# Performance work log

Measured on AMD Instinct MI355X. Metric: run time of the kernel, lower is better.

The kernel has to match this reference:

```python
import jax, jax.numpy as jnp
import numpy as np

D_IN, D_H, D_G, H, B = 512, 256, 128, 8, 4096
EPS_LN = 1e-6
EPS_STD = 1e-6


def setup_inputs() -> dict:
    key = jax.random.key(0)
    ks = jax.random.split(key, 4)
    x = jax.random.normal(ks[0], (B, D_IN), dtype=jnp.float32)
    # Dense params (flax kernel layout: (in, out)), lecun-normal-ish init
    Wh = jax.random.normal(ks[1], (D_IN, D_H), dtype=jnp.float32) / np.sqrt(D_IN)
    bh = jnp.zeros((D_H,), dtype=jnp.float32)
    Wz1 = jax.random.normal(ks[2], (D_IN, H * D_H), dtype=jnp.float32) / np.sqrt(D_IN)
    Wz2 = jax.random.normal(ks[3], (D_IN, H * D_G), dtype=jnp.float32) / np.sqrt(D_IN)
    ln_scale = jnp.ones((D_H,), dtype=jnp.float32)
    ln_bias = jnp.zeros((D_H,), dtype=jnp.float32)
    return {"x": x, "Wh": Wh, "bh": bh, "Wz1": Wz1, "Wz2": Wz2,
            "ln_scale": ln_scale, "ln_bias": ln_bias}


def _layer_norm(a, scale, bias):
    mu = jnp.mean(a, axis=-1, keepdims=True)
    var = jnp.var(a, axis=-1, keepdims=True)
    return (a - mu) * jax.lax.rsqrt(var + EPS_LN) * scale + bias


def reference(x, Wh, bh, Wz1, Wz2, ln_scale, ln_bias):
    sz_b = x.shape[0]
    # h: (B, d_h)
    h = _layer_norm(jax.nn.relu(x @ Wh + bh), ln_scale, ln_bias)
    z1 = (x @ Wz1).reshape(sz_b, H, D_H)   # (B, H, d_h)
    z2 = (x @ Wz2).reshape(sz_b, H, D_G)   # (B, H, d_g)
    # w = z2^T @ z1 over heads: (B, d_g, d_h)
    w = jnp.einsum('bhg,bhd->bgd', z2, z1)
    # per-row standardization (population std, ddof=0) + tanh
    mu = jnp.mean(w, axis=-1, keepdims=True)
    sd = jnp.std(w, axis=-1, keepdims=True)
    w = jnp.tanh((w - mu) / (sd + EPS_STD))
    # y = w @ h: (B, d_g)
    y = jnp.einsum('bgd,bd->bg', w, h)
    return h, y
```

## Files before the change

kernel.cpp:

```cpp
#include <hip/hip_runtime.h>
#include <hip/hip_bf16.h>
#include <cstdint>

#define BATCH 4096
#define DIN   512
#define DH    256
#define DG    128
#define NH    8
#define NTOT  3328
#define S2    264

typedef __bf16 bf16x8 __attribute__((ext_vector_type(8)));
typedef float  f32x4  __attribute__((ext_vector_type(4)));

__device__ __forceinline__ unsigned short f2bf(float f) {
    union { float f; uint32_t u; } v; v.f = f;
    uint32_t u = v.u;
    u += 0x7fffu + ((u >> 16) & 1u);
    return (unsigned short)(u >> 16);
}
__device__ __forceinline__ float bf2f(unsigned short s) {
    union { uint32_t u; float f; } v; v.u = ((uint32_t)s) << 16;
    return v.f;
}

__device__ __forceinline__ void async16(const unsigned short* g, unsigned short* l) {
    __builtin_amdgcn_global_load_lds(
        (const __attribute__((address_space(1))) unsigned int*)(uintptr_t)g,
        (__attribute__((address_space(3))) unsigned int*)(uintptr_t)l,
        16, 0, 0);
}

__global__ __launch_bounds__(256) void prep_kernel(const float* __restrict__ x,
                                                   const float* __restrict__ Wh,
                                                   const float* __restrict__ Wz1,
                                                   const float* __restrict__ Wz2,
                                                   unsigned short* __restrict__ xb,
                                                   unsigned short* __restrict__ Wt) {
    __shared__ float tile[32][33];
    int bid = blockIdx.x;
    int t = threadIdx.x;
    if (bid < 2048) {
        int i = (bid * 256 + t) * 4;
        float4 v = *(const float4*)(x + i);
        ushort4 o;
        o.x = f2bf(v.x); o.y = f2bf(v.y); o.z = f2bf(v.z); o.w = f2bf(v.w);
        *(ushort4*)(xb + i) = o;
        return;
    }
    int b2 = bid - 2048;
    int n0 = (b2 % 104) * 32;
    int k0 = (b2 / 104) * 32;
    const float* W; int ldn, nl;
    if (n0 < 256)       { W = Wh;  ldn = 256;  nl = n0; }
    else if (n0 < 2304) { W = Wz1; ldn = 2048; nl = n0 - 256; }
    else                { W = Wz2; ldn = 1024; nl = n0 - 2304; }
    int tx = t & 31, ty = t >> 5;
    #pragma unroll
    for (int i = 0; i < 4; i++) {
        int kk = ty + i * 8;
        tile[kk][tx] = W[(size_t)(k0 + kk) * ldn + nl + tx];
    }
    __syncthreads();
    #pragma unroll
    for (int i = 0; i < 4; i++) {
        int nn = ty + i * 8;
        Wt[(size_t)(n0 + nn) * 512 + k0 + tx] = f2bf(tile[tx][nn]);
    }
}

__global__ __launch_bounds__(256) void gemm_kernel(const unsigned short* __restrict__ xb,
                                                   const unsigned short* __restrict__ Wt,
                                                   unsigned short* __restrict__ Zb) {
    __shared__ unsigned short As[128 * 64];
    __shared__ unsigned short Bs[128 * 64];
    const int m0 = blockIdx.y * 128;
    const int n0 = blockIdx.x * 128;
    const int t = threadIdx.x;
    const int w = t >> 6, lane = t & 63;
    const int wm = (w >> 1) * 64, wn = (w & 1) * 64;
    const int lrow = lane & 15, q = lane >> 4;

    f32x4 acc[4][4] = {};

    for (int k0 = 0; k0 < DIN; k0 += 64) {
        __syncthreads();
        #pragma unroll
        for (int j = 0; j < 4; j++) {
            int gidx = (w * 4 + j) * 64 + lane;
            int row = gidx >> 3, slot = gidx & 7;
            int src = slot ^ (row & 7);
            const unsigned short* ga = xb + (size_t)(m0 + row) * DIN + k0 + src * 8;
            const unsigned short* gb = Wt + (size_t)(n0 + row) * DIN + k0 + src * 8;
            async16(ga, As + (w * 4 + j) * 512);
            async16(gb, Bs + (w * 4 + j) * 512);
        }
        __syncthreads();
        #pragma unroll
        for (int ks = 0; ks < 2; ks++) {
            bf16x8 af[4], bfr[4];
            #pragma unroll
            for (int i = 0; i < 4; i++) {
                int row = wm + i * 16 + lrow;
                int phys = (ks * 4 + q) ^ (row & 7);
                af[i] = *reinterpret_cast<const bf16x8*>(As + row * 64 + phys * 8);
            }
            #pragma unroll
            for (int j = 0; j < 4; j++) {
                int row = wn + j * 16 + lrow;
                int phys = (ks * 4 + q) ^ (row & 7);
                bfr[j] = *reinterpret_cast<const bf16x8*>(Bs + row * 64 + phys * 8);
            }
            #pragma unroll
            for (int i = 0; i < 4; i++)
                #pragma unroll
                for (int j = 0; j < 4; j++)
                    acc[i][j] = __builtin_amdgcn_mfma_f32_16x16x32_bf16(af[i], bfr[j], acc[i][j], 0, 0, 0);
        }
    }
    #pragma unroll
    for (int i = 0; i < 4; i++)
        #pragma unroll
        for (int j = 0; j < 4; j++) {
            int col = n0 + wn + j * 16 + lrow;
            int rbase = m0 + wm + i * 16 + q * 4;
            #pragma unroll
            for (int r = 0; r < 4; r++)
                Zb[(size_t)(rbase + r) * NTOT + col] = f2bf(acc[i][j][r]);
        }
}

__global__ __launch_bounds__(256) void attn_kernel(const unsigned short* __restrict__ Zb,
                                                   const float* __restrict__ bh,
                                                   const float* __restrict__ lns,
                                                   const float* __restrict__ lnb,
                                                   float* __restrict__ h_out,
                                                   float* __restrict__ y_out) {
    __shared__ unsigned short z1s[16 * S2];
    __shared__ unsigned short z2s[NH * DG];
    __shared__ unsigned short z1cb[DH * 8];
    __shared__ unsigned short z2A[DG * 8];
    __shared__ unsigned short zpad[8];
    __shared__ float hs[DH];
    __shared__ float GL[9][9];
    __shared__ float red[4][3];
    const int b = blockIdx.x;
    const int t = threadIdx.x;
    const int wv = t >> 6, lane = t & 63;
    const int lrow = lane & 15, q = lane >> 4;
    const unsigned short* Zrow = Zb + (size_t)b * NTOT;

    {
        uint4 v1 = *(const uint4*)(Zrow + 256 + t * 8);
        *(uint4*)(z1s + (t >> 5) * S2 + (t & 31) * 8) = v1;
        if (t < 128) {
            uint4 v2 = *(const uint4*)(Zrow + 2304 + t * 8);
            *(uint4*)(z2s + t * 8) = v2;
        }
        z1s[8 * S2 + t] = 0x3F80;
        if (t < 8) zpad[t] = 0;
    }
    float v = fmaxf(bf2f(Zrow[t]) + bh[t], 0.0f);
    float s = v, sq = v * v;
    #pragma unroll
    for (int m = 32; m >= 1; m >>= 1) {
        s  += __shfl_xor(s,  m, 64);
        sq += __shfl_xor(sq, m, 64);
    }
    if (lane == 0) { red[wv][0] = s; red[wv][1] = sq; }
    __syncthreads();

    if (wv == 3) {
        f32x4 g = {};
        #pragma unroll
        for (int ks = 0; ks < 8; ks++) {
            bf16x8 fr = *reinterpret_cast<const bf16x8*>(z1s + lrow * S2 + ks * 32 + q * 8);
            g = __builtin_amdgcn_mfma_f32_16x16x32_bf16(fr, fr, g, 0, 0, 0);
        }
        #pragma unroll
        for (int r = 0; r < 4; r++) {
            int row = q * 4 + r;
            if (row < 9 && lrow < 9) GL[row][lrow] = g[r];
        }
    }
    {
        float ss = red[0][0] + red[1][0] + red[2][0] + red[3][0];
        float qq = red[0][1] + red[1][1] + red[2][1] + red[3][1];
        float mu  = ss * (1.0f / 256.0f);
        float var = qq * (1.0f / 256.0f) - mu * mu;
        float hval = (v - mu) * rsqrtf(var + 1e-6f) * lns[t] + lnb[t];
        hs[t] = hval;
        h_out[(size_t)b * DH + t] = hval;
        float hp = hval;
        #pragma unroll
        for (int m = 32; m >= 1; m >>= 1) hp += __shfl_xor(hp, m, 64);
        if (lane == 0) red[wv][2] = hp;
    }
    __syncthreads();

    {
        unsigned short pk[8];
        #pragma unroll
        for (int h = 0; h < NH; h++) {
            float c = bf2f(z1s[h * S2 + t]) - GL[h][8] * (1.0f / 256.0f);
            pk[h] = f2bf(c);
        }
        ushort4 lo = {pk[0], pk[1], pk[2], pk[3]};
        ushort4 hi = {pk[4], pk[5], pk[6], pk[7]};
        *(ushort4*)(z1cb + t * 8)     = lo;
        *(ushort4*)(z1cb + t * 8 + 4) = hi;
    }
    if (t < DG) {
        float z2g[NH];
        #pragma unroll
        for (int h = 0; h < NH; h++) z2g[h] = bf2f(z2s[h * DG + t]);
        float mug = 0.f, qg = 0.f;
        #pragma unroll
        for (int h = 0; h < NH; h++) {
            mug += z2g[h] * GL[h][8];
            float inn = 0.f;
            #pragma unroll
            for (int h2 = 0; h2 < NH; h2++) inn += z2g[h2] * GL[h][h2];
            qg += z2g[h] * inn;
        }
        mug *= (1.0f / 256.0f);
        qg  *= (1.0f / 256.0f);
        float vg = fmaxf(qg - mug * mug, 0.0f);
        float A = 2.0f * 1.4426950408889634f / (sqrtf(vg) + 1e-6f);
        unsigned short pk[8];
        #pragma unroll
        for (int h = 0; h < NH; h++) pk[h] = f2bf(z2g[h] * A);
        ushort4 lo = {pk[0], pk[1], pk[2], pk[3]};
        ushort4 hi = {pk[4], pk[5], pk[6], pk[7]};
        *(ushort4*)(z2A + t * 8)     = lo;
        *(ushort4*)(z2A + t * 8 + 4) = hi;
    }
    __syncthreads();

    const unsigned short* bptr = (q == 0) ? (z1cb + lrow * 8) : zpad;
    const int binc = (q == 0) ? 128 : 0;
    bf16x8 af[2];
    #pragma unroll
    for (int gt = 0; gt < 2; gt++) {
        const unsigned short* aptr = (q == 0) ? (z2A + (wv * 32 + gt * 16 + lrow) * 8) : zpad;
        af[gt] = *reinterpret_cast<const bf16x8*>(aptr);
    }
    float hv[16];
    #pragma unroll
    for (int dt = 0; dt < 16; dt++) hv[dt] = hs[dt * 16 + lrow];

    f32x4 czero = {};
    float yn[2][4] = {};
    #pragma unroll 4
    for (int dt = 0; dt < 16; dt++) {
        bf16x8 bfr = *reinterpret_cast<const bf16x8*>(bptr + dt * binc);
        #pragma unroll
        for (int gt = 0; gt < 2; gt++) {
            f32x4 c = __builtin_amdgcn_mfma_f32_16x16x32_bf16(af[gt], bfr, czero, 0, 0, 0);
            #pragma unroll
            for (int r = 0; r < 4; r++) {
                float e = __builtin_amdgcn_exp2f(c[r]);
                yn[gt][r] = fmaf(hv[dt], __builtin_amdgcn_rcpf(e + 1.0f), yn[gt][r]);
            }
        }
    }
    #pragma unroll
    for (int m = 1; m <= 8; m <<= 1)
        #pragma unroll
        for (int gt = 0; gt < 2; gt++)
            #pragma unroll
            for (int r = 0; r < 4; r++)
                yn[gt][r] += __shfl_xor(yn[gt][r], m, 64);
    if (lrow == 0) {
        float Hsum = red[0][2] + red[1][2] + red[2][2] + red[3][2];
        #pragma unroll
        for (int gt = 0; gt < 2; gt++)
            #pragma unroll
            for (int r = 0; r < 4; r++)
                y_out[(size_t)b * DG + wv * 32 + gt * 16 + q * 4 + r] = Hsum - 2.0f * yn[gt][r];
    }
}

extern "C" void kernel_launch(void* const* d_in, const int* in_sizes, int n_in,
                              void* d_out, int out_size, void* d_ws, size_t ws_size,
                              hipStream_t stream) {
    const float* x   = (const float*)d_in[0];
    const float* Wh  = (const float*)d_in[1];
    const float* bh  = (const float*)d_in[2];
    const float* Wz1 = (const float*)d_in[3];
    const float* Wz2 = (const float*)d_in[4];
    const float* lns = (const float*)d_in[5];
    const float* lnb = (const float*)d_in[6];
    float* h_out = (float*)d_out;
    float* y_out = h_out + (size_t)BATCH * DH;

    char* ws = (char*)d_ws;
    unsigned short* Zb = (unsigned short*)ws;
    unsigned short* xb = (unsigned short*)(ws + 27262976);
    unsigned short* Wt = (unsigned short*)(ws + 31457280);

    prep_kernel<<<3712, 256, 0, stream>>>(x, Wh, Wz1, Wz2, xb, Wt);
    gemm_kernel<<<dim3(NTOT / 128, BATCH / 128), 256, 0, stream>>>(xb, Wt, Zb);
    attn_kernel<<<BATCH, 256, 0, stream>>>(Zb, bh, lns, lnb, h_out, y_out);
}
```

Baseline: 144.1 us.

## Process eight batch rows per attention block with one wave per row pair

New measurement: 142.3 us. No clear change (-1.2%).

```diff
diff --git a/kernel.cpp b/kernel.cpp
--- a/kernel.cpp
+++ b/kernel.cpp
@@ -8,7 +8,9 @@
 #define DG    128
 #define NH    8
 #define NTOT  3328
-#define S2    264
+#define RPB   8
+#define SH    264
+#define RREG  (9 * SH)
 
 typedef __bf16 bf16x8 __attribute__((ext_vector_type(8)));
 typedef float  f32x4  __attribute__((ext_vector_type(4)));
@@ -130,154 +132,214 @@
         }
 }
 
-__global__ __launch_bounds__(256) void attn_kernel(const unsigned short* __restrict__ Zb,
-                                                   const float* __restrict__ bh,
-                                                   const float* __restrict__ lns,
-                                                   const float* __restrict__ lnb,
-                                                   float* __restrict__ h_out,
-                                                   float* __restrict__ y_out) {
-    __shared__ unsigned short z1s[16 * S2];
-    __shared__ unsigned short z2s[NH * DG];
-    __shared__ unsigned short z1cb[DH * 8];
-    __shared__ unsigned short z2A[DG * 8];
-    __shared__ unsigned short zpad[8];
-    __shared__ float hs[DH];
-    __shared__ float GL[9][9];
-    __shared__ float red[4][3];
-    const int b = blockIdx.x;
+__global__ __launch_bounds__(256, 2) void attn_kernel(const unsigned short* __restrict__ Zb,
+                                                      const float* __restrict__ bh,
+                                                      const float* __restrict__ lns,
+                                                      const float* __restrict__ lnb,
+                                                      float* __restrict__ h_out,
+                                                      float* __restrict__ y_out) {
+    __shared__ __align__(16) unsigned short z1a[RPB * RREG + 7 * SH];
+    __shared__ __align__(16) unsigned short z2b[RPB * 1024];
+    __shared__ __align__(16) float hsr[RPB][DH];
+    __shared__ float GLr[RPB][9][9];
+    __shared__ float redH[RPB];
+    __shared__ __align__(16) unsigned short zpad[8];
+    const int b0 = blockIdx.x * RPB;
     const int t = threadIdx.x;
     const int wv = t >> 6, lane = t & 63;
     const int lrow = lane & 15, q = lane >> 4;
-    const unsigned short* Zrow = Zb + (size_t)b * NTOT;
+
+    #pragma unroll
+    for (int r = 0; r < RPB; r++) {
+        const unsigned short* Zr = Zb + (size_t)(b0 + r) * NTOT;
+        uint4 v = *(const uint4*)(Zr + 256 + t * 8);
+        *(uint4*)(z1a + r * RREG + (t >> 5) * SH + (t & 31) * 8) = v;
+        z1a[r * RREG + 8 * SH + t] = 0x3F80;
+    }
+    #pragma unroll
+    for (int i = 0; i < 4; i++) {
+        int idx = i * 256 + t;
+        int r = idx >> 7, c = idx & 127;
+        uint4 v = *(const uint4*)(Zb + (size_t)(b0 + r) * NTOT + 2304 + c * 8);
+        *(uint4*)(z2b + r * 1024 + c * 8) = v;
+    }
+    if (t < 8) zpad[t] = 0;
 
     {
-        uint4 v1 = *(const uint4*)(Zrow + 256 + t * 8);
-        *(uint4*)(z1s + (t >> 5) * S2 + (t & 31) * 8) = v1;
-        if (t < 128) {
-            uint4 v2 = *(const uint4*)(Zrow + 2304 + t * 8);
-            *(uint4*)(z2s + t * 8) = v2;
-        }
-        z1s[8 * S2 + t] = 0x3F80;
-        if (t < 8) zpad[t] = 0;
-    }
-    float v = fmaxf(bf2f(Zrow[t]) + bh[t], 0.0f);
-    float s = v, sq = v * v;
-    #pragma unroll
-    for (int m = 32; m >= 1; m >>= 1) {
-        s  += __shfl_xor(s,  m, 64);
-        sq += __shfl_xor(sq, m, 64);
-    }
-    if (lane == 0) { red[wv][0] = s; red[wv][1] = sq; }
-    __syncthreads();
-
-    if (wv == 3) {
+        int r = t >> 5, d0 = (t & 31) * 8;
+        const unsigned short* Zr = Zb + (size_t)(b0 + r) * NTOT;
+        uint4 hp4 = *(const uint4*)(Zr + d0);
+        unsigned short hu[8];
+        *(uint4*)hu = hp4;
+        float4 ba = *(const float4*)(bh + d0);
+        float4 bb = *(const float4*)(bh + d0 + 4);
+        float vv[8];
+        vv[0] = fmaxf(bf2f(hu[0]) + ba.x, 0.f); vv[1] = fmaxf(bf2f(hu[1]) + ba.y, 0.f);
+        vv[2] = fmaxf(bf2f(hu[2]) + ba.z, 0.f); vv[3] = fmaxf(bf2f(hu[3]) + ba.w, 0.f);
+        vv[4] = fmaxf(bf2f(hu[4]) + bb.x, 0.f); vv[5] = fmaxf(bf2f(hu[5]) + bb.y, 0.f);
+        vv[6] = fmaxf(bf2f(hu[6]) + bb.z, 0.f); vv[7] = fmaxf(bf2f(hu[7]) + bb.w, 0.f);
+        float s = 0.f, sq = 0.f;
+        #pragma unroll
+        for (int i = 0; i < 8; i++) { s += vv[i]; sq += vv[i] * vv[i]; }
+        #pragma unroll
+        for (int m = 16; m >= 1; m >>= 1) {
+            s  += __shfl_xor(s,  m, 64);
+            sq += __shfl_xor(sq, m, 64);
+        }
+        float mu  = s * (1.0f / 256.0f);
+        float var = sq * (1.0f / 256.0f) - mu * mu;
+        float rs = rsqrtf(var + 1e-6f);
+        float4 la = *(const float4*)(lns + d0);
+        float4 lb = *(const float4*)(lns + d0 + 4);
+        float4 oa = *(const float4*)(lnb + d0);
+        float4 ob = *(const float4*)(lnb + d0 + 4);
+        float hvv[8];
+        hvv[0] = (vv[0] - mu) * rs * la.x + oa.x; hvv[1] = (vv[1] - mu) * rs * la.y + oa.y;
+        hvv[2] = (vv[2] - mu) * rs * la.z + oa.z; hvv[3] = (vv[3] - mu) * rs * la.w + oa.w;
+        hvv[4] = (vv[4] - mu) * rs * lb.x + ob.x; hvv[5] = (vv[5] - mu) * rs * lb.y + ob.y;
+        hvv[6] = (vv[6] - mu) * rs * lb.z + ob.z; hvv[7] = (vv[7] - mu) * rs * lb.w + ob.w;
+        *(float4*)(&hsr[r][d0])     = float4{hvv[0], hvv[1], hvv[2], hvv[3]};
+        *(float4*)(&hsr[r][d0 + 4]) = float4{hvv[4], hvv[5], hvv[6], hvv[7]};
+        float* ho = h_out + (size_t)(b0 + r) * DH + d0;
+        *(float4*)ho       = float4{hvv[0], hvv[1], hvv[2], hvv[3]};
+        *(float4*)(ho + 4) = float4{hvv[4], hvv[5], hvv[6], hvv[7]};
+        float hp = 0.f;
+        #pragma unroll
+        for (int i = 0; i < 8; i++) hp += hvv[i];
+        #pragma unroll
+        for (int m = 16; m >= 1; m >>= 1) hp += __shfl_xor(hp, m, 64);
+        if ((t & 31) == 0) redH[r] = hp;
+    }
+    __syncthreads();
+
+    #pragma unroll
+    for (int rr = 0; rr < 2; rr++) {
+        int r = wv * 2 + rr;
         f32x4 g = {};
         #pragma unroll
         for (int ks = 0; ks < 8; ks++) {
-            bf16x8 fr = *reinterpret_cast<const bf16x8*>(z1s + lrow * S2 + ks * 32 + q * 8);
+            bf16x8 fr = *reinterpret_cast<const bf16x8*>(z1a + r * RREG + lrow * SH + ks * 32 + q * 8);
             g = __builtin_amdgcn_mfma_f32_16x16x32_bf16(fr, fr, g, 0, 0, 0);
         }
         #pragma unroll
-        for (int r = 0; r < 4; r++) {
-            int row = q * 4 + r;
-            if (row < 9 && lrow < 9) GL[row][lrow] = g[r];
-        }
-    }
+        for (int i = 0; i < 4; i++) {
+            int crow = q * 4 + i;
+            if (crow < 9 && lrow < 9) GLr[r][crow][lrow] = g[i];
+        }
+    }
+    uint32_t pr[8][4];
     {
-        float ss = red[0][0] + red[1][0] + red[2][0] + red[3][0];
-        float qq = red[0][1] + red[1][1] + red[2][1] + red[3][1];
-        float mu  = ss * (1.0f / 256.0f);
-        float var = qq * (1.0f / 256.0f) - mu * mu;
-        float hval = (v - mu) * rsqrtf(var + 1e-6f) * lns[t] + lnb[t];
-        hs[t] = hval;
-        h_out[(size_t)b * DH + t] = hval;
-        float hp = hval;
-        #pragma unroll
-        for (int m = 32; m >= 1; m >>= 1) hp += __shfl_xor(hp, m, 64);
-        if (lane == 0) red[wv][2] = hp;
+        int r = t >> 5, la = t & 31;
+        float mh[8];
+        #pragma unroll
+        for (int h = 0; h < NH; h++) mh[h] = GLr[r][h][8] * (1.0f / 256.0f);
+        #pragma unroll
+        for (int jj = 0; jj < 8; jj++) {
+            int d = la + 32 * jj;
+            #pragma unroll
+            for (int h2 = 0; h2 < 4; h2++) {
+                float c0 = bf2f(z1a[r * RREG + (2 * h2) * SH + d])     - mh[2 * h2];
+                float c1 = bf2f(z1a[r * RREG + (2 * h2 + 1) * SH + d]) - mh[2 * h2 + 1];
+                pr[jj][h2] = (uint32_t)f2bf(c0) | ((uint32_t)f2bf(c1) << 16);
+            }
+        }
     }
     __syncthreads();
 
     {
-        unsigned short pk[8];
+        int r = t >> 5, la = t & 31;
+        #pragma unroll
+        for (int jj = 0; jj < 8; jj++) {
+            int d = la + 32 * jj;
+            *(uint4*)(z1a + r * RREG + d * 8) = uint4{pr[jj][0], pr[jj][1], pr[jj][2], pr[jj][3]};
+        }
+    }
+    uint32_t ps[4][4];
+    #pragma unroll
+    for (int i = 0; i < 4; i++) {
+        int idx = i * 256 + t;
+        int r = idx >> 7, g = idx & 127;
+        float z2g[NH];
+        #pragma unroll
+        for (int h = 0; h < NH; h++) z2g[h] = bf2f(z2b[r * 1024 + h * 128 + g]);
+        float mug = 0.f, qg = 0.f;
         #pragma unroll
         for (int h = 0; h < NH; h++) {
-            float c = bf2f(z1s[h * S2 + t]) - GL[h][8] * (1.0f / 256.0f);
-            pk[h] = f2bf(c);
-        }
-        ushort4 lo = {pk[0], pk[1], pk[2], pk[3]};
-        ushort4 hi = {pk[4], pk[5], pk[6], pk[7]};
-        *(ushort4*)(z1cb + t * 8)     = lo;
-        *(ushort4*)(z1cb + t * 8 + 4) = hi;
-    }
-    if (t < DG) {
-        float z2g[NH];
-        #pragma unroll
-        for (int h = 0; h < NH; h++) z2g[h] = bf2f(z2s[h * DG + t]);
-        float mug = 0.f, qg = 0.f;
-        #pragma unroll
-        for (int h = 0; h < NH; h++) {
-            mug += z2g[h] * GL[h][8];
+            mug += z2g[h] * GLr[r][h][8];
             float inn = 0.f;
             #pragma unroll
-            for (int h2 = 0; h2 < NH; h2++) inn += z2g[h2] * GL[h][h2];
+            for (int h2 = 0; h2 < NH; h2++) inn += z2g[h2] * GLr[r][h][h2];
             qg += z2g[h] * inn;
         }
         mug *= (1.0f / 256.0f);
         qg  *= (1.0f / 256.0f);
         float vg = fmaxf(qg - mug * mug, 0.0f);
         float A = 2.0f * 1.4426950408889634f / (sqrtf(vg) + 1e-6f);
-        unsigned short pk[8];
-        #pragma unroll
-        for (int h = 0; h < NH; h++) pk[h] = f2bf(z2g[h] * A);
-        ushort4 lo = {pk[0], pk[1], pk[2], pk[3]};
-        ushort4 hi = {pk[4], pk[5], pk[6], pk[7]};
-        *(ushort4*)(z2A + t * 8)     = lo;
-        *(ushort4*)(z2A + t * 8 + 4) = hi;
-    }
-    __syncthreads();
-
-    const unsigned short* bptr = (q == 0) ? (z1cb + lrow * 8) : zpad;
+        #pragma unroll
+        for (int h2 = 0; h2 < 4; h2++)
+            ps[i][h2] = (uint32_t)f2bf(z2g[2 * h2] * A) | ((uint32_t)f2bf(z2g[2 * h2 + 1] * A) << 16);
+    }
+    __syncthreads();
+
+    #pragma unroll
+    for (int i = 0; i < 4; i++) {
+        int idx = i * 256 + t;
+        int r = idx >> 7, g = idx & 127;
+        *(uint4*)(z2b + r * 1024 + g * 8) = uint4{ps[i][0], ps[i][1], ps[i][2], ps[i][3]};
+    }
+    __syncthreads();
+
+    const int ra = wv * 2, rb = wv * 2 + 1;
+    const unsigned short* bpA = (q == 0) ? (z1a + ra * RREG + lrow * 8) : zpad;
+    const unsigned short* bpB = (q == 0) ? (z1a + rb * RREG + lrow * 8) : zpad;
     const int binc = (q == 0) ? 128 : 0;
-    bf16x8 af[2];
-    #pragma unroll
-    for (int gt = 0; gt < 2; gt++) {
-        const unsigned short* aptr = (q == 0) ? (z2A + (wv * 32 + gt * 16 + lrow) * 8) : zpad;
-        af[gt] = *reinterpret_cast<const bf16x8*>(aptr);
-    }
-    float hv[16];
-    #pragma unroll
-    for (int dt = 0; dt < 16; dt++) hv[dt] = hs[dt * 16 + lrow];
-
+    bf16x8 afA[8], afB[8];
+    #pragma unroll
+    for (int gt = 0; gt < 8; gt++) {
+        const unsigned short* pa = (q == 0) ? (z2b + ra * 1024 + (gt * 16 + lrow) * 8) : zpad;
+        const unsigned short* pb = (q == 0) ? (z2b + rb * 1024 + (gt * 16 + lrow) * 8) : zpad;
+        afA[gt] = *reinterpret_cast<const bf16x8*>(pa);
+        afB[gt] = *reinterpret_cast<const bf16x8*>(pb);
+    }
     f32x4 czero = {};
-    float yn[2][4] = {};
-    #pragma unroll 4
+    float ynA[8][4] = {}, ynB[8][4] = {};
+    #pragma unroll 2
     for (int dt = 0; dt < 16; dt++) {
-        bf16x8 bfr = *reinterpret_cast<const bf16x8*>(bptr + dt * binc);
-        #pragma unroll
-        for (int gt = 0; gt < 2; gt++) {
-            f32x4 c = __builtin_amdgcn_mfma_f32_16x16x32_bf16(af[gt], bfr, czero, 0, 0, 0);
-            #pragma unroll
-            for (int r = 0; r < 4; r++) {
-                float e = __builtin_amdgcn_exp2f(c[r]);
-                yn[gt][r] = fmaf(hv[dt], __builtin_amdgcn_rcpf(e + 1.0f), yn[gt][r]);
+        bf16x8 bA = *reinterpret_cast<const bf16x8*>(bpA + dt * binc);
+        bf16x8 bB = *reinterpret_cast<const bf16x8*>(bpB + dt * binc);
+        float hvA = hsr[ra][dt * 16 + lrow];
+        float hvB = hsr[rb][dt * 16 + lrow];
+        #pragma unroll
+        for (int gt = 0; gt < 8; gt++) {
+            f32x4 cA = __builtin_amdgcn_mfma_f32_16x16x32_bf16(afA[gt], bA, czero, 0, 0, 0);
+            f32x4 cB = __builtin_amdgcn_mfma_f32_16x16x32_bf16(afB[gt], bB, czero, 0, 0, 0);
+            #pragma unroll
+            for (int r4 = 0; r4 < 4; r4++) {
+                float eA = __builtin_amdgcn_exp2f(cA[r4]);
+                ynA[gt][r4] = fmaf(hvA, __builtin_amdgcn_rcpf(eA + 1.0f), ynA[gt][r4]);
+                float eB = __builtin_amdgcn_exp2f(cB[r4]);
+                ynB[gt][r4] = fmaf(hvB, __builtin_amdgcn_rcpf(eB + 1.0f), ynB[gt][r4]);
             }
         }
     }
     #pragma unroll
     for (int m = 1; m <= 8; m <<= 1)
         #pragma unroll
-        for (int gt = 0; gt < 2; gt++)
-            #pragma unroll
-            for (int r = 0; r < 4; r++)
-                yn[gt][r] += __shfl_xor(yn[gt][r], m, 64);
+        for (int gt = 0; gt < 8; gt++)
+            #pragma unroll
+            for (int r4 = 0; r4 < 4; r4++) {
+                ynA[gt][r4] += __shfl_xor(ynA[gt][r4], m, 64);
+                ynB[gt][r4] += __shfl_xor(ynB[gt][r4], m, 64);
+            }
     if (lrow == 0) {
-        float Hsum = red[0][2] + red[1][2] + red[2][2] + red[3][2];
-        #pragma unroll
-        for (int gt = 0; gt < 2; gt++)
-            #pragma unroll
-            for (int r = 0; r < 4; r++)
-                y_out[(size_t)b * DG + wv * 32 + gt * 16 + q * 4 + r] = Hsum - 2.0f * yn[gt][r];
+        float HsA = redH[ra], HsB = redH[rb];
+        #pragma unroll
+        for (int gt = 0; gt < 8; gt++)
+            #pragma unroll
+            for (int r4 = 0; r4 < 4; r4++) {
+                y_out[(size_t)(b0 + ra) * DG + gt * 16 + q * 4 + r4] = HsA - 2.0f * ynA[gt][r4];
+                y_out[(size_t)(b0 + rb) * DG + gt * 16 + q * 4 + r4] = HsB - 2.0f * ynB[gt][r4];
+            }
     }
 }
 
@@ -301,5 +363,5 @@
 
     prep_kernel<<<3712, 256, 0, stream>>>(x, Wh, Wz1, Wz2, xb, Wt);
     gemm_kernel<<<dim3(NTOT / 128, BATCH / 128), 256, 0, stream>>>(xb, Wt, Zb);
-    attn_kernel<<<BATCH, 256, 0, stream>>>(Zb, bh, lns, lnb, h_out, y_out);
-}
+    attn_kernel<<<BATCH / RPB, 256, 0, stream>>>(Zb, bh, lns, lnb, h_out, y_out);
+}
```

## Process two batch rows per block in attn kernel with reworked work split

Applied to the files above, without the earlier changes.

After: 145.6 us. Within noise of the previous version (+1.0%).

```diff
diff --git a/kernel.cpp b/kernel.cpp
--- a/kernel.cpp
+++ b/kernel.cpp
@@ -8,7 +8,9 @@
 #define DG    128
 #define NH    8
 #define NTOT  3328
-#define S2    264
+#define RPB   2
+#define SH    264
+#define RREG  (9 * SH)
 
 typedef __bf16 bf16x8 __attribute__((ext_vector_type(8)));
 typedef float  f32x4  __attribute__((ext_vector_type(4)));
@@ -130,154 +132,175 @@
         }
 }
 
-__global__ __launch_bounds__(256) void attn_kernel(const unsigned short* __restrict__ Zb,
-                                                   const float* __restrict__ bh,
-                                                   const float* __restrict__ lns,
-                                                   const float* __restrict__ lnb,
-                                                   float* __restrict__ h_out,
-                                                   float* __restrict__ y_out) {
-    __shared__ unsigned short z1s[16 * S2];
-    __shared__ unsigned short z2s[NH * DG];
-    __shared__ unsigned short z1cb[DH * 8];
-    __shared__ unsigned short z2A[DG * 8];
-    __shared__ unsigned short zpad[8];
-    __shared__ float hs[DH];
-    __shared__ float GL[9][9];
-    __shared__ float red[4][3];
-    const int b = blockIdx.x;
+__global__ __launch_bounds__(256, 8) void attn_kernel(const unsigned short* __restrict__ Zb,
+                                                      const float* __restrict__ bh,
+                                                      const float* __restrict__ lns,
+                                                      const float* __restrict__ lnb,
+                                                      float* __restrict__ h_out,
+                                                      float* __restrict__ y_out) {
+    __shared__ __align__(16) unsigned short z1a[RPB * RREG + 7 * SH];
+    __shared__ __align__(16) unsigned short z2b[RPB * 1024];
+    __shared__ __align__(16) float hsr[RPB][DH];
+    __shared__ float GLr[RPB][9][9];
+    __shared__ float redH[RPB];
+    __shared__ __align__(16) unsigned short zpad[8];
+    const int b0 = blockIdx.x * RPB;
     const int t = threadIdx.x;
     const int wv = t >> 6, lane = t & 63;
     const int lrow = lane & 15, q = lane >> 4;
-    const unsigned short* Zrow = Zb + (size_t)b * NTOT;
-
+
+    #pragma unroll
+    for (int r = 0; r < RPB; r++) {
+        uint4 v = *(const uint4*)(Zb + (size_t)(b0 + r) * NTOT + 256 + t * 8);
+        *(uint4*)(z1a + r * RREG + (t >> 5) * SH + (t & 31) * 8) = v;
+        z1a[r * RREG + 8 * SH + t] = 0x3F80;
+    }
     {
-        uint4 v1 = *(const uint4*)(Zrow + 256 + t * 8);
-        *(uint4*)(z1s + (t >> 5) * S2 + (t & 31) * 8) = v1;
-        if (t < 128) {
-            uint4 v2 = *(const uint4*)(Zrow + 2304 + t * 8);
-            *(uint4*)(z2s + t * 8) = v2;
-        }
-        z1s[8 * S2 + t] = 0x3F80;
-        if (t < 8) zpad[t] = 0;
-    }
-    float v = fmaxf(bf2f(Zrow[t]) + bh[t], 0.0f);
-    float s = v, sq = v * v;
-    #pragma unroll
-    for (int m = 32; m >= 1; m >>= 1) {
-        s  += __shfl_xor(s,  m, 64);
-        sq += __shfl_xor(sq, m, 64);
-    }
-    if (lane == 0) { red[wv][0] = s; red[wv][1] = sq; }
-    __syncthreads();
-
-    if (wv == 3) {
+        int r = t >> 7, c = t & 127;
+        uint4 v = *(const uint4*)(Zb + (size_t)(b0 + r) * NTOT + 2304 + c * 8);
+        *(uint4*)(z2b + r * 1024 + c * 8) = v;
+    }
+    if (t < 8) zpad[t] = 0;
+
+    if (wv < 2) {
+        int r = wv, d0 = lane * 4;
+        const unsigned short* Zr = Zb + (size_t)(b0 + r) * NTOT;
+        ushort4 hu = *(const ushort4*)(Zr + d0);
+        float4 bv = *(const float4*)(bh + d0);
+        float vv[4];
+        vv[0] = fmaxf(bf2f(hu.x) + bv.x, 0.f);
+        vv[1] = fmaxf(bf2f(hu.y) + bv.y, 0.f);
+        vv[2] = fmaxf(bf2f(hu.z) + bv.z, 0.f);
+        vv[3] = fmaxf(bf2f(hu.w) + bv.w, 0.f);
+        float s = vv[0] + vv[1] + vv[2] + vv[3];
+        float sq = vv[0] * vv[0] + vv[1] * vv[1] + vv[2] * vv[2] + vv[3] * vv[3];
+        #pragma unroll
+        for (int m = 32; m >= 1; m >>= 1) {
+            s  += __shfl_xor(s,  m, 64);
+            sq += __shfl_xor(sq, m, 64);
+        }
+        float mu  = s * (1.0f / 256.0f);
+        float var = sq * (1.0f / 256.0f) - mu * mu;
+        float rs = rsqrtf(var + 1e-6f);
+        float4 lv = *(const float4*)(lns + d0);
+        float4 ov = *(const float4*)(lnb + d0);
+        float hv0 = (vv[0] - mu) * rs * lv.x + ov.x;
+        float hv1 = (vv[1] - mu) * rs * lv.y + ov.y;
+        float hv2 = (vv[2] - mu) * rs * lv.z + ov.z;
+        float hv3 = (vv[3] - mu) * rs * lv.w + ov.w;
+        *(float4*)(&hsr[r][d0]) = float4{hv0, hv1, hv2, hv3};
+        *(float4*)(h_out + (size_t)(b0 + r) * DH + d0) = float4{hv0, hv1, hv2, hv3};
+        float hp = hv0 + hv1 + hv2 + hv3;
+        #pragma unroll
+        for (int m = 32; m >= 1; m >>= 1) hp += __shfl_xor(hp, m, 64);
+        if (lane == 0) redH[r] = hp;
+    }
+    __syncthreads();
+
+    if (wv < 2) {
+        int r = wv;
         f32x4 g = {};
         #pragma unroll
         for (int ks = 0; ks < 8; ks++) {
-            bf16x8 fr = *reinterpret_cast<const bf16x8*>(z1s + lrow * S2 + ks * 32 + q * 8);
+            bf16x8 fr = *reinterpret_cast<const bf16x8*>(z1a + r * RREG + lrow * SH + ks * 32 + q * 8);
             g = __builtin_amdgcn_mfma_f32_16x16x32_bf16(fr, fr, g, 0, 0, 0);
         }
         #pragma unroll
-        for (int r = 0; r < 4; r++) {
-            int row = q * 4 + r;
-            if (row < 9 && lrow < 9) GL[row][lrow] = g[r];
-        }
-    }
+        for (int i = 0; i < 4; i++) {
+            int crow = q * 4 + i;
+            if (crow < 9 && lrow < 9) GLr[r][crow][lrow] = g[i];
+        }
+    }
+    const int sr = t >> 7, sg = t & 127;
+    float z2g[NH];
+    #pragma unroll
+    for (int h = 0; h < NH; h++) z2g[h] = bf2f(z2b[sr * 1024 + h * 128 + sg]);
+    __syncthreads();
+
+    uint32_t pr[2][4];
     {
-        float ss = red[0][0] + red[1][0] + red[2][0] + red[3][0];
-        float qq = red[0][1] + red[1][1] + red[2][1] + red[3][1];
-        float mu  = ss * (1.0f / 256.0f);
-        float var = qq * (1.0f / 256.0f) - mu * mu;
-        float hval = (v - mu) * rsqrtf(var + 1e-6f) * lns[t] + lnb[t];
-        hs[t] = hval;
-        h_out[(size_t)b * DH + t] = hval;
-        float hp = hval;
-        #pragma unroll
-        for (int m = 32; m >= 1; m >>= 1) hp += __shfl_xor(hp, m, 64);
-        if (lane == 0) red[wv][2] = hp;
-    }
-    __syncthreads();
-
+        float mh[NH];
+        #pragma unroll
+        for (int h = 0; h < NH; h++) mh[h] = GLr[sr][h][8] * (1.0f / 256.0f);
+        #pragma unroll
+        for (int it = 0; it < 2; it++) {
+            int d = (t & 127) + it * 128;
+            #pragma unroll
+            for (int h2 = 0; h2 < 4; h2++) {
+                float c0 = bf2f(z1a[sr * RREG + (2 * h2) * SH + d])     - mh[2 * h2];
+                float c1 = bf2f(z1a[sr * RREG + (2 * h2 + 1) * SH + d]) - mh[2 * h2 + 1];
+                pr[it][h2] = (uint32_t)f2bf(c0) | ((uint32_t)f2bf(c1) << 16);
+            }
+        }
+    }
+    uint32_t ps[4];
     {
-        unsigned short pk[8];
+        float mug = 0.f, qg = 0.f;
         #pragma unroll
         for (int h = 0; h < NH; h++) {
-            float c = bf2f(z1s[h * S2 + t]) - GL[h][8] * (1.0f / 256.0f);
-            pk[h] = f2bf(c);
-        }
-        ushort4 lo = {pk[0], pk[1], pk[2], pk[3]};
-        ushort4 hi = {pk[4], pk[5], pk[6], pk[7]};
-        *(ushort4*)(z1cb + t * 8)     = lo;
-        *(ushort4*)(z1cb + t * 8 + 4) = hi;
-    }
-    if (t < DG) {
-        float z2g[NH];
-        #pragma unroll
-        for (int h = 0; h < NH; h++) z2g[h] = bf2f(z2s[h * DG + t]);
-        float mug = 0.f, qg = 0.f;
-        #pragma unroll
-        for (int h = 0; h < NH; h++) {
-            mug += z2g[h] * GL[h][8];
+            mug += z2g[h] * GLr[sr][h][8];
             float inn = 0.f;
             #pragma unroll
-            for (int h2 = 0; h2 < NH; h2++) inn += z2g[h2] * GL[h][h2];
+            for (int h2 = 0; h2 < NH; h2++) inn += z2g[h2] * GLr[sr][h][h2];
             qg += z2g[h] * inn;
         }
         mug *= (1.0f / 256.0f);
         qg  *= (1.0f / 256.0f);
         float vg = fmaxf(qg - mug * mug, 0.0f);
         float A = 2.0f * 1.4426950408889634f / (sqrtf(vg) + 1e-6f);
-        unsigned short pk[8];
-        #pragma unroll
-        for (int h = 0; h < NH; h++) pk[h] = f2bf(z2g[h] * A);
-        ushort4 lo = {pk[0], pk[1], pk[2], pk[3]};
-        ushort4 hi = {pk[4], pk[5], pk[6], pk[7]};
-        *(ushort4*)(z2A + t * 8)     = lo;
-        *(ushort4*)(z2A + t * 8 + 4) = hi;
-    }
-    __syncthreads();
-
-    const unsigned short* bptr = (q == 0) ? (z1cb + lrow * 8) : zpad;
+        #pragma unroll
+        for (int h2 = 0; h2 < 4; h2++)
+            ps[h2] = (uint32_t)f2bf(z2g[2 * h2] * A) | ((uint32_t)f2bf(z2g[2 * h2 + 1] * A) << 16);
+    }
+    __syncthreads();
+
+    #pragma unroll
+    for (int it = 0; it < 2; it++) {
+        int d = (t & 127) + it * 128;
+        *(uint4*)(z1a + sr * RREG + d * 8) = uint4{pr[it][0], pr[it][1], pr[it][2], pr[it][3]};
+    }
+    *(uint4*)(z2b + sr * 1024 + sg * 8) = uint4{ps[0], ps[1], ps[2], ps[3]};
+    __syncthreads();
+
+    const int row = wv >> 1, gtb = (wv & 1) * 4;
+    const unsigned short* bp = (q == 0) ? (z1a + row * RREG + lrow * 8) : zpad;
     const int binc = (q == 0) ? 128 : 0;
-    bf16x8 af[2];
-    #pragma unroll
-    for (int gt = 0; gt < 2; gt++) {
-        const unsigned short* aptr = (q == 0) ? (z2A + (wv * 32 + gt * 16 + lrow) * 8) : zpad;
-        af[gt] = *reinterpret_cast<const bf16x8*>(aptr);
-    }
-    float hv[16];
-    #pragma unroll
-    for (int dt = 0; dt < 16; dt++) hv[dt] = hs[dt * 16 + lrow];
-
+    bf16x8 af[4];
+    #pragma unroll
+    for (int gt = 0; gt < 4; gt++) {
+        const unsigned short* pa = (q == 0) ? (z2b + row * 1024 + ((gtb + gt) * 16 + lrow) * 8) : zpad;
+        af[gt] = *reinterpret_cast<const bf16x8*>(pa);
+    }
     f32x4 czero = {};
-    float yn[2][4] = {};
+    float yn[4][4] = {};
     #pragma unroll 4
     for (int dt = 0; dt < 16; dt++) {
-        bf16x8 bfr = *reinterpret_cast<const bf16x8*>(bptr + dt * binc);
-        #pragma unroll
-        for (int gt = 0; gt < 2; gt++) {
+        bf16x8 bfr = *reinterpret_cast<const bf16x8*>(bp + dt * binc);
+        float hv = hsr[row][dt * 16 + lrow];
+        #pragma unroll
+        for (int gt = 0; gt < 4; gt++) {
             f32x4 c = __builtin_amdgcn_mfma_f32_16x16x32_bf16(af[gt], bfr, czero, 0, 0, 0);
             #pragma unroll
-            for (int r = 0; r < 4; r++) {
-                float e = __builtin_amdgcn_exp2f(c[r]);
-                yn[gt][r] = fmaf(hv[dt], __builtin_amdgcn_rcpf(e + 1.0f), yn[gt][r]);
+            for (int r4 = 0; r4 < 4; r4++) {
+                float e = __builtin_amdgcn_exp2f(c[r4]);
+                yn[gt][r4] = fmaf(hv, __builtin_amdgcn_rcpf(e + 1.0f), yn[gt][r4]);
             }
         }
     }
     #pragma unroll
     for (int m = 1; m <= 8; m <<= 1)
         #pragma unroll
-        for (int gt = 0; gt < 2; gt++)
-            #pragma unroll
-            for (int r = 0; r < 4; r++)
-                yn[gt][r] += __shfl_xor(yn[gt][r], m, 64);
+        for (int gt = 0; gt < 4; gt++)
+            #pragma unroll
+            for (int r4 = 0; r4 < 4; r4++)
+                yn[gt][r4] += __shfl_xor(yn[gt][r4], m, 64);
     if (lrow == 0) {
-        float Hsum = red[0][2] + red[1][2] + red[2][2] + red[3][2];
-        #pragma unroll
-        for (int gt = 0; gt < 2; gt++)
-            #pragma unroll
-            for (int r = 0; r < 4; r++)
-                y_out[(size_t)b * DG + wv * 32 + gt * 16 + q * 4 + r] = Hsum - 2.0f * yn[gt][r];
+        float Hs = redH[row];
+        #pragma unroll
+        for (int gt = 0; gt < 4; gt++)
+            #pragma unroll
+            for (int r4 = 0; r4 < 4; r4++)
+                y_out[(size_t)(b0 + row) * DG + (gtb + gt) * 16 + q * 4 + r4] = Hs - 2.0f * yn[gt][r4];
     }
 }
 
@@ -301,5 +324,5 @@
 
     prep_kernel<<<3712, 256, 0, stream>>>(x, Wh, Wz1, Wz2, xb, Wt);
     gemm_kernel<<<dim3(NTOT / 128, BATCH / 128), 256, 0, stream>>>(xb, Wt, Zb);
-    attn_kernel<<<BATCH, 256, 0, stream>>>(Zb, bh, lns, lnb, h_out, y_out);
-}
+    attn_kernel<<<BATCH / RPB, 256, 0, stream>>>(Zb, bh, lns, lnb, h_out, y_out);
+}
```
